# Kernel tuning notes

Measured on AMD Instinct MI355X. Metric: run time of the kernel, lower is better.

Reference implementation:

```python
import jax, jax.numpy as jnp
import numpy as np

BN_EPS = 1e-5
CUT_THRESH = 1e-3  # cut_conv1 zeroes a channel plane if its abs-max < 0.001


def setup_inputs() -> dict:
    key = jax.random.key(0)
    k1, k2, k3 = jax.random.split(key, 3)
    B, Cin, Cout, H, W, K = 32, 32, 32, 192, 192, 3
    return {
        "x": jax.random.normal(k1, (B, Cin, H, W), dtype=jnp.float32),
        "conv_w": jax.random.normal(k2, (Cout, Cin, K, K), dtype=jnp.float32) * 0.05,
        "conv_b": jax.random.normal(k3, (Cout,), dtype=jnp.float32) * 0.05,
        "gamma": jnp.ones((Cout,), dtype=jnp.float32),
        "beta": jnp.zeros((Cout,), dtype=jnp.float32),
        "run_mean": jnp.zeros((Cout,), dtype=jnp.float32),
        "run_var": jnp.ones((Cout,), dtype=jnp.float32),
    }


def reference(x, conv_w, conv_b, gamma, beta, run_mean, run_var):
    # Conv2d, stride 1, padding 1 (NCHW / OIHW)
    y = jax.lax.conv_general_dilated(
        x, conv_w, window_strides=(1, 1), padding=((1, 1), (1, 1)),
        dimension_numbers=("NCHW", "OIHW", "NCHW"))
    y = y + conv_b[None, :, None, None]
    # BatchNorm2d (inference form with running stats)
    inv_std = gamma * jax.lax.rsqrt(run_var + BN_EPS)
    y = (y - run_mean[None, :, None, None]) * inv_std[None, :, None, None] \
        + beta[None, :, None, None]
    # ReLU
    y = jnp.maximum(y, 0.0)
    # cut_conv1: per (batch, channel) abs-max; zero whole plane if below threshold.
    # Vectorized replacement of the original B*C Python loop.
    chan_absmax = jnp.max(jnp.abs(y), axis=(2, 3), keepdims=True)  # [B, C, 1, 1]
    return jnp.where(chan_absmax < CUT_THRESH, jnp.zeros_like(y), y)
```

## Files before the change

### kernel.cpp

```cpp
#include <hip/hip_runtime.h>

typedef short short8 __attribute__((ext_vector_type(8)));
typedef float f32x4 __attribute__((ext_vector_type(4)));

#define BN_EPS 1e-5f
#define CUT_THRESH 1e-3f

#define WS_COEF 18432
#define WS_PART 18688

__device__ __forceinline__ unsigned short f2bf(float f) {
  unsigned u = __float_as_uint(f);
  u += 0x7FFFu + ((u >> 16) & 1u);
  return (unsigned short)(u >> 16);
}

__device__ __forceinline__ void gload_lds16(const void* g, void* l) {
  __builtin_amdgcn_global_load_lds(
      (const __attribute__((address_space(1))) unsigned int*)g,
      (__attribute__((address_space(3))) unsigned int*)l, 16, 0, 0);
}

__global__ void prep_kernel(const float* __restrict__ wgt,
                            const float* __restrict__ bias,
                            const float* __restrict__ gamma,
                            const float* __restrict__ beta,
                            const float* __restrict__ rmean,
                            const float* __restrict__ rvar,
                            unsigned short* __restrict__ wbf,
                            float* __restrict__ coef) {
  int tid = blockIdx.x * 256 + threadIdx.x;
  if (tid < 9216) {
    int co = tid / 288;
    int rem = tid - co * 288;
    int ci = rem / 9;
    int kk = rem - ci * 9;
    int oct = ((ci >> 3) ^ ((co >> 1) & 3)) << 3;
    wbf[(kk * 32 + co) * 32 + oct + (ci & 7)] = f2bf(wgt[tid]);
  }
  if (tid < 32) {
    float s = gamma[tid] * rsqrtf(rvar[tid] + BN_EPS);
    coef[tid] = s;
    coef[32 + tid] = (bias[tid] - rmean[tid]) * s + beta[tid];
  }
}

__global__ __launch_bounds__(256, 3) void conv_bn_relu_kernel(
    const float* __restrict__ x,
    const unsigned short* __restrict__ wbf,
    const float* __restrict__ coef,
    float* __restrict__ out,
    float* __restrict__ part) {
  __shared__ unsigned short lx[10 * 34 * 32];
  __shared__ unsigned short lw[9 * 32 * 32];

  int bid = blockIdx.x;
  int orig = (bid & 7) * 576 + (bid >> 3);
  int b = orig / 144;
  int t = orig - b * 144;
  int tr = t / 6, tc = t - tr * 6;
  int r0 = tr * 8, c0 = tc * 32;
  int tid = threadIdx.x;

  {
    const short8* wsrc = reinterpret_cast<const short8*>(wbf);
    short8* wdst = reinterpret_cast<short8*>(lw);
#pragma unroll
    for (int r = 0; r < 4; ++r) gload_lds16(wsrc + r * 256 + tid, wdst + r * 256 + tid);
    if (tid < 128) gload_lds16(wsrc + 1024 + tid, wdst + 1024 + tid);
  }

  const float* xb = x + b * (32 * 192 * 192);
  int m80 = tid;
  m80 = (m80 >= 160) ? m80 - 160 : m80;
  m80 = (m80 >= 80) ? m80 - 80 : m80;

  float fv[6][8];
  int lofs[6];
  int okm[6];
#pragma unroll
  for (int r = 0; r < 6; ++r) {
    int id = (r < 5) ? (r * 256 + tid) : (1280 + m80);
    int g = id & 3;
    int p = id >> 2;
    int h = p / 34;
    int w = p - h * 34;
    int gh = r0 - 1 + h, gw = c0 - 1 + w;
    okm[r] = (((unsigned)gh < 192u) && ((unsigned)gw < 192u)) ? -1 : 0;
    int ghc = min(max(gh, 0), 191);
    int gwc = min(max(gw, 0), 191);
    const float* src = xb + (g * 8) * 36864 + ghc * 192 + gwc;
#pragma unroll
    for (int j = 0; j < 8; ++j) fv[r][j] = src[j * 36864];
    lofs[r] = p * 32 + ((g ^ ((w >> 1) & 3)) << 3);
  }
  __builtin_amdgcn_sched_barrier(0);

#pragma unroll
  for (int r = 0; r < 6; ++r) {
    unsigned pk[4];
#pragma unroll
    for (int q = 0; q < 4; ++q) {
      float f0 = okm[r] ? fv[r][2 * q] : 0.f;
      float f1 = okm[r] ? fv[r][2 * q + 1] : 0.f;
      unsigned a = __float_as_uint(f0) + 0x8000u;
      unsigned c = __float_as_uint(f1) + 0x8000u;
      pk[q] = (a >> 16) | (c & 0xffff0000u);
    }
    short8 v;
    reinterpret_cast<unsigned*>(&v)[0] = pk[0];
    reinterpret_cast<unsigned*>(&v)[1] = pk[1];
    reinterpret_cast<unsigned*>(&v)[2] = pk[2];
    reinterpret_cast<unsigned*>(&v)[3] = pk[3];
    *reinterpret_cast<short8*>(&lx[lofs[r]]) = v;
  }

  int lane = tid & 63;
  int wv = tid >> 6;
  int l15 = lane & 15;
  int lg = lane >> 4;

  f32x4 scl[2], sft[2];
#pragma unroll
  for (int m = 0; m < 2; ++m) {
    scl[m] = *reinterpret_cast<const f32x4*>(coef + m * 16 + lg * 4);
    sft[m] = *reinterpret_cast<const f32x4*>(coef + 32 + m * 16 + lg * 4);
  }

  __syncthreads();

  int aswz = (lg ^ ((l15 >> 1) & 3)) << 3;
  f32x4 acc[2][4] = {};

#pragma unroll
  for (int s = 0; s < 9; ++s) {
    const int kh = s / 3, kw = s - kh * 3;
    short8 A0 = *reinterpret_cast<const short8*>(&lw[(s * 32 + l15) * 32 + aswz]);
    short8 A1 = *reinterpret_cast<const short8*>(&lw[(s * 32 + 16 + l15) * 32 + aswz]);
#pragma unroll
    for (int n = 0; n < 4; ++n) {
      int hl = 2 * wv + (n >> 1) + kh;
      int wl = ((n & 1) << 4) + l15 + kw;
      short8 Bf = *reinterpret_cast<const short8*>(
          &lx[(hl * 34 + wl) * 32 + ((lg ^ ((wl >> 1) & 3)) << 3)]);
      acc[0][n] = __builtin_amdgcn_mfma_f32_16x16x32_bf16(A0, Bf, acc[0][n], 0, 0, 0);
      acc[1][n] = __builtin_amdgcn_mfma_f32_16x16x32_bf16(A1, Bf, acc[1][n], 0, 0, 0);
    }
  }

  const int HW = 192 * 192;
  float* ob = out + b * 32 * HW;
  float pmax[2][4];
#pragma unroll
  for (int m = 0; m < 2; ++m)
#pragma unroll
    for (int j = 0; j < 4; ++j) pmax[m][j] = 0.f;

#pragma unroll
  for (int m = 0; m < 2; ++m)
#pragma unroll
    for (int n = 0; n < 4; ++n) {
      int gr = r0 + 2 * wv + (n >> 1);
      int gc = c0 + ((n & 1) << 4) + l15;
#pragma unroll
      for (int j = 0; j < 4; ++j) {
        int co = m * 16 + lg * 4 + j;
        float v = fmaxf(acc[m][n][j] * scl[m][j] + sft[m][j], 0.f);
        __builtin_nontemporal_store(v, &ob[co * HW + gr * 192 + gc]);
        pmax[m][j] = fmaxf(pmax[m][j], v);
      }
    }

#pragma unroll
  for (int m = 0; m < 2; ++m)
#pragma unroll
    for (int j = 0; j < 4; ++j) {
      float v = pmax[m][j];
      v = fmaxf(v, __shfl_xor(v, 1, 16));
      v = fmaxf(v, __shfl_xor(v, 2, 16));
      v = fmaxf(v, __shfl_xor(v, 4, 16));
      v = fmaxf(v, __shfl_xor(v, 8, 16));
      if (l15 == 0) {
        int co = m * 16 + lg * 4 + j;
        __builtin_nontemporal_store(v, &part[((size_t)b * 32 + co) * 576 + t * 4 + wv]);
      }
    }
}

__global__ __launch_bounds__(256) void cut_kernel(float* __restrict__ out,
                                                  const float* __restrict__ part) {
  __shared__ float r4[4];
  int p = blockIdx.x;
  const float* pp = part + (size_t)p * 576;
  float m = 0.f;
  for (int i = threadIdx.x; i < 576; i += 256) m = fmaxf(m, pp[i]);
#pragma unroll
  for (int k = 1; k < 64; k <<= 1) m = fmaxf(m, __shfl_xor(m, k, 64));
  if ((threadIdx.x & 63) == 0) r4[threadIdx.x >> 6] = m;
  __syncthreads();
  m = fmaxf(fmaxf(r4[0], r4[1]), fmaxf(r4[2], r4[3]));
  if (m >= CUT_THRESH) return;
  float* base = out + (size_t)p * 36864;
  for (int i = threadIdx.x; i < 36864; i += 256) base[i] = 0.f;
}

extern "C" void kernel_launch(void* const* d_in, const int* in_sizes, int n_in,
                              void* d_out, int out_size, void* d_ws, size_t ws_size,
                              hipStream_t stream) {
  const float* x     = (const float*)d_in[0];
  const float* wgt   = (const float*)d_in[1];
  const float* bias  = (const float*)d_in[2];
  const float* gamma = (const float*)d_in[3];
  const float* beta  = (const float*)d_in[4];
  const float* rmean = (const float*)d_in[5];
  const float* rvar  = (const float*)d_in[6];
  float* out = (float*)d_out;

  unsigned short* wbf  = (unsigned short*)d_ws;
  float*          coef = (float*)((char*)d_ws + WS_COEF);
  float*          part = (float*)((char*)d_ws + WS_PART);

  prep_kernel<<<36, 256, 0, stream>>>(wgt, bias, gamma, beta, rmean, rvar, wbf, coef);
  conv_bn_relu_kernel<<<4608, 256, 0, stream>>>(x, wbf, coef, out, part);
  cut_kernel<<<1024, 256, 0, stream>>>(out, part);
}
```

Measured before the change: 76.70 us.

## Load input halo tile with float4 vector loads and specialize interior tiles

The input tile staging is rewritten so each thread loads four consecutive columns per channel with 16-byte vector loads, instead of scalar per-pixel loads. The LDS row stride is widened from 34 to 36 columns so each row splits evenly into four-column groups. Interior tiles take a branch-free path with no clamping, while edge tiles shift and zero lanes to handle padding. This cuts the number of global load instructions and address calculations, at the cost of more registers, more complex packing logic, and some wasted halo columns.

After: 77.77 us. No clear change (+1.4%).

```diff
diff --git a/kernel.cpp b/kernel.cpp
--- a/kernel.cpp
+++ b/kernel.cpp
@@ -45,13 +45,86 @@
   }
 }
 
+struct Task {
+  f32x4 L[8];
+  int pbase;
+  int g, k01, k23, dcase;
+  unsigned rm;
+};
+
+template <bool INT>
+__device__ __forceinline__ void issue_task(int id, const float* __restrict__ xb,
+                                           int r0, int c0, Task& T) {
+  int g = id & 3;
+  int pq = id >> 2;
+  int h = pq / 9;
+  int q = pq - h * 9;
+  int gh = r0 - 1 + h;
+  int B = c0 - 1 + 4 * q;
+  int ghc, Bc;
+  if (INT) {
+    ghc = gh; Bc = B; T.rm = 1u; T.dcase = 0;
+  } else {
+    T.rm = ((unsigned)gh < 192u) ? 1u : 0u;
+    ghc = min(max(gh, 0), 191);
+    T.dcase = (B < 0) ? 1 : ((B > 188) ? 2 : 0);
+    Bc = min(max(B, 0), 188);
+  }
+  const float* src = xb + (g * 8) * 36864 + ghc * 192 + Bc;
+#pragma unroll
+  for (int j = 0; j < 8; ++j)
+    T.L[j] = *reinterpret_cast<const f32x4*>(src + j * 36864);
+  T.pbase = (h * 36 + 4 * q) * 32;
+  T.g = g;
+  T.k01 = (2 * q) & 3;
+  T.k23 = (2 * q + 1) & 3;
+}
+
+template <bool INT>
+__device__ __forceinline__ void pack_task(const Task& T,
+                                          unsigned short* __restrict__ lx) {
+#pragma unroll
+  for (int wi = 0; wi < 4; ++wi) {
+    const int key = (wi < 2) ? 0 : 1;
+    unsigned pk[4];
+#pragma unroll
+    for (int c = 0; c < 4; ++c) {
+      float e0, e1;
+      if (INT) {
+        e0 = T.L[2 * c][wi];
+        e1 = T.L[2 * c + 1][wi];
+      } else {
+        float n0 = T.L[2 * c][wi], n1 = T.L[2 * c + 1][wi];
+        float l0 = (wi == 0) ? 0.f : T.L[2 * c][wi == 0 ? 0 : wi - 1];
+        float l1 = (wi == 0) ? 0.f : T.L[2 * c + 1][wi == 0 ? 0 : wi - 1];
+        float r0_ = (wi == 0) ? T.L[2 * c][3] : 0.f;
+        float r1_ = (wi == 0) ? T.L[2 * c + 1][3] : 0.f;
+        e0 = (T.dcase == 0) ? n0 : ((T.dcase == 1) ? l0 : r0_);
+        e1 = (T.dcase == 0) ? n1 : ((T.dcase == 1) ? l1 : r1_);
+        e0 = T.rm ? e0 : 0.f;
+        e1 = T.rm ? e1 : 0.f;
+      }
+      unsigned a = __float_as_uint(e0) + 0x8000u;
+      unsigned cc = __float_as_uint(e1) + 0x8000u;
+      pk[c] = __builtin_amdgcn_perm(cc, a, 0x07060302u);
+    }
+    short8 v;
+    reinterpret_cast<unsigned*>(&v)[0] = pk[0];
+    reinterpret_cast<unsigned*>(&v)[1] = pk[1];
+    reinterpret_cast<unsigned*>(&v)[2] = pk[2];
+    reinterpret_cast<unsigned*>(&v)[3] = pk[3];
+    int k = key ? T.k23 : T.k01;
+    *reinterpret_cast<short8*>(&lx[T.pbase + wi * 32 + ((T.g ^ k) << 3)]) = v;
+  }
+}
+
 __global__ __launch_bounds__(256, 3) void conv_bn_relu_kernel(
     const float* __restrict__ x,
     const unsigned short* __restrict__ wbf,
     const float* __restrict__ coef,
     float* __restrict__ out,
     float* __restrict__ part) {
-  __shared__ unsigned short lx[10 * 34 * 32];
+  __shared__ unsigned short lx[10 * 36 * 32];
   __shared__ unsigned short lw[9 * 32 * 32];
 
   int bid = blockIdx.x;
@@ -71,48 +144,20 @@
   }
 
   const float* xb = x + b * (32 * 192 * 192);
-  int m80 = tid;
-  m80 = (m80 >= 160) ? m80 - 160 : m80;
-  m80 = (m80 >= 80) ? m80 - 80 : m80;
-
-  float fv[6][8];
-  int lofs[6];
-  int okm[6];
-#pragma unroll
-  for (int r = 0; r < 6; ++r) {
-    int id = (r < 5) ? (r * 256 + tid) : (1280 + m80);
-    int g = id & 3;
-    int p = id >> 2;
-    int h = p / 34;
-    int w = p - h * 34;
-    int gh = r0 - 1 + h, gw = c0 - 1 + w;
-    okm[r] = (((unsigned)gh < 192u) && ((unsigned)gw < 192u)) ? -1 : 0;
-    int ghc = min(max(gh, 0), 191);
-    int gwc = min(max(gw, 0), 191);
-    const float* src = xb + (g * 8) * 36864 + ghc * 192 + gwc;
-#pragma unroll
-    for (int j = 0; j < 8; ++j) fv[r][j] = src[j * 36864];
-    lofs[r] = p * 32 + ((g ^ ((w >> 1) & 3)) << 3);
-  }
-  __builtin_amdgcn_sched_barrier(0);
-
-#pragma unroll
-  for (int r = 0; r < 6; ++r) {
-    unsigned pk[4];
-#pragma unroll
-    for (int q = 0; q < 4; ++q) {
-      float f0 = okm[r] ? fv[r][2 * q] : 0.f;
-      float f1 = okm[r] ? fv[r][2 * q + 1] : 0.f;
-      unsigned a = __float_as_uint(f0) + 0x8000u;
-      unsigned c = __float_as_uint(f1) + 0x8000u;
-      pk[q] = (a >> 16) | (c & 0xffff0000u);
-    }
-    short8 v;
-    reinterpret_cast<unsigned*>(&v)[0] = pk[0];
-    reinterpret_cast<unsigned*>(&v)[1] = pk[1];
-    reinterpret_cast<unsigned*>(&v)[2] = pk[2];
-    reinterpret_cast<unsigned*>(&v)[3] = pk[3];
-    *reinterpret_cast<short8*>(&lx[lofs[r]]) = v;
+  bool has2 = tid < 104;
+  Task T0, T1;
+  if (tr >= 1 && tr <= 22 && tc >= 1 && tc <= 4) {
+    issue_task<true>(tid, xb, r0, c0, T0);
+    if (has2) issue_task<true>(256 + tid, xb, r0, c0, T1);
+    __builtin_amdgcn_sched_barrier(0);
+    pack_task<true>(T0, lx);
+    if (has2) pack_task<true>(T1, lx);
+  } else {
+    issue_task<false>(tid, xb, r0, c0, T0);
+    if (has2) issue_task<false>(256 + tid, xb, r0, c0, T1);
+    __builtin_amdgcn_sched_barrier(0);
+    pack_task<false>(T0, lx);
+    if (has2) pack_task<false>(T1, lx);
   }
 
   int lane = tid & 63;
@@ -142,7 +187,7 @@
       int hl = 2 * wv + (n >> 1) + kh;
       int wl = ((n & 1) << 4) + l15 + kw;
       short8 Bf = *reinterpret_cast<const short8*>(
-          &lx[(hl * 34 + wl) * 32 + ((lg ^ ((wl >> 1) & 3)) << 3)]);
+          &lx[(hl * 36 + wl) * 32 + ((lg ^ ((wl >> 1) & 3)) << 3)]);
       acc[0][n] = __builtin_amdgcn_mfma_f32_16x16x32_bf16(A0, Bf, acc[0][n], 0, 0, 0);
       acc[1][n] = __builtin_amdgcn_mfma_f32_16x16x32_bf16(A1, Bf, acc[1][n], 0, 0, 0);
     }
```
